# Kernel tuning notes

Hardware: AMD Instinct MI355X
Metric: run time of the kernel (lower is better)

Reference implementation:

```python
import jax, jax.numpy as jnp
import numpy as np

N = 100000   # nodes
E = 1600000  # directed edges
D_IN, D_HID, D_OUT, N_CLS = 128, 256, 128, 10
EPS = 1e-5


def gcn_conv(x, W, b, src, dst, n):
    # PyG GCNConv: h = XW, add self loops, sym-normalize, scatter-add to dst, + bias
    h = x @ W
    loop = jnp.arange(n)
    src_f = jnp.concatenate([src, loop])
    dst_f = jnp.concatenate([dst, loop])
    deg = jax.ops.segment_sum(jnp.ones(src_f.shape[0], h.dtype), dst_f, num_segments=n)
    dinv = jnp.where(deg > 0, jax.lax.rsqrt(deg), jnp.zeros_like(deg))
    norm = dinv[src_f] * dinv[dst_f]                    # [E+N]
    out = jax.ops.segment_sum(h[src_f] * norm[:, None], dst_f, num_segments=n)
    return out + b


def batchnorm(x, gamma, beta):
    # training-mode BatchNorm1d (batch statistics, biased variance)
    mu = x.mean(0)
    var = x.var(0)
    return gamma * (x - mu) * jax.lax.rsqrt(var + EPS) + beta


def setup_inputs() -> dict:
    key = jax.random.key(0)
    ks = jax.random.split(key, 12)
    x = jax.random.normal(ks[0], (N, D_IN), jnp.float32)
    edge_index = jax.random.randint(ks[1], (2, E), 0, N, dtype=jnp.int64)
    def lin(k, fi, fo):
        s = 1.0 / np.sqrt(fi)
        return jax.random.uniform(k, (fi, fo), jnp.float32, -s, s)
    return {
        "x": x, "edge_index": edge_index,
        "W1": lin(ks[2], D_IN, D_HID), "b1": jnp.zeros(D_HID, jnp.float32),
        "g1": jnp.ones(D_HID, jnp.float32), "beta1": jnp.zeros(D_HID, jnp.float32),
        "W2": lin(ks[3], D_HID, D_HID), "b2": jnp.zeros(D_HID, jnp.float32),
        "g2": jnp.ones(D_HID, jnp.float32), "beta2": jnp.zeros(D_HID, jnp.float32),
        "W3": lin(ks[4], D_HID, D_OUT), "b3": jnp.zeros(D_OUT, jnp.float32),
        "g3": jnp.ones(D_OUT, jnp.float32), "beta3": jnp.zeros(D_OUT, jnp.float32),
        "Wout": lin(ks[5], D_OUT, N_CLS), "bout": jnp.zeros(N_CLS, jnp.float32),
    }


def reference(x, edge_index, W1, b1, g1, beta1, W2, b2, g2, beta2,
              W3, b3, g3, beta3, Wout, bout):
    src, dst = edge_index[0], edge_index[1]
    h = jax.nn.relu(batchnorm(gcn_conv(x, W1, b1, src, dst, N), g1, beta1))
    h = jax.nn.relu(batchnorm(gcn_conv(h, W2, b2, src, dst, N), g2, beta2))
    h = jax.nn.relu(batchnorm(gcn_conv(h, W3, b3, src, dst, N), g3, beta3))
    return h @ Wout + bout
```

## Files before the change

### kernel.cpp

```cpp
#include <hip/hip_runtime.h>
#include <hip/hip_fp16.h>
#include <cstdint>
#include <cstddef>

#define EPS_BN 1e-5f
#define NSLICE 16
#define NCHUNK 16

static inline int cdiv(int a, int b) { return (a + b - 1) / b; }

using half8   = __attribute__((ext_vector_type(8))) _Float16;
using floatx4 = __attribute__((ext_vector_type(4))) float;

__device__ __forceinline__ float atomAddF(float* p, float v) {
    return unsafeAtomicAdd(p, v);
}


__global__ __launch_bounds__(256) void k_hist(const int* __restrict__ dst, int E,
                                              int NBLK, int NBUCK, int* __restrict__ H) {
    __shared__ int h[256];
    int t = threadIdx.x;
    h[t] = 0;
    __syncthreads();
    int base = blockIdx.x * 4096;
#pragma unroll
    for (int j = 0; j < 16; ++j) {
        int e = base + j * 256 + t;
        if (e < E) atomicAdd(&h[dst[e] >> 9], 1);
    }
    __syncthreads();
    if (t < NBUCK) H[t * NBLK + blockIdx.x] = h[t];
}

__global__ __launch_bounds__(256) void k_scan_reduce(const int* __restrict__ in, int m,
                                                     int* __restrict__ bsum) {
    int base = blockIdx.x * 1024;
    int t = threadIdx.x;
    int s = 0;
#pragma unroll
    for (int i = 0; i < 4; ++i) {
        int idx = base + t * 4 + i;
        if (idx < m) s += in[idx];
    }
    __shared__ int sm[256];
    sm[t] = s;
    __syncthreads();
    for (int off = 128; off > 0; off >>= 1) {
        if (t < off) sm[t] += sm[t + off];
        __syncthreads();
    }
    if (t == 0) bsum[blockIdx.x] = sm[0];
}

__global__ void k_scan_bsum(int* __restrict__ bsum, int nb) {
    if (threadIdx.x == 0 && blockIdx.x == 0) {
        int acc = 0;
        for (int i = 0; i < nb; ++i) { int v = bsum[i]; bsum[i] = acc; acc += v; }
    }
}

__global__ __launch_bounds__(256) void k_scan_final(const int* __restrict__ in, int m,
                                                    const int* __restrict__ bsum,
                                                    int* __restrict__ outS) {
    int base = blockIdx.x * 1024;
    int t = threadIdx.x;
    int v[4];
    int s = 0;
#pragma unroll
    for (int i = 0; i < 4; ++i) {
        int idx = base + t * 4 + i;
        v[i] = (idx < m) ? in[idx] : 0;
        s += v[i];
    }
    __shared__ int sm[256];
    sm[t] = s;
    __syncthreads();
    for (int off = 1; off < 256; off <<= 1) {
        int x = (t >= off) ? sm[t - off] : 0;
        __syncthreads();
        sm[t] += x;
        __syncthreads();
    }
    int excl = sm[t] - s + bsum[blockIdx.x];
#pragma unroll
    for (int i = 0; i < 4; ++i) {
        int idx = base + t * 4 + i;
        if (idx < m) { outS[idx] = excl; excl += v[i]; }
    }
}

__global__ __launch_bounds__(256) void k_bucket(const int* __restrict__ src,
                                                const int* __restrict__ dst, int E,
                                                int NBLK, int NBUCK,
                                                const int* __restrict__ S,
                                                unsigned* __restrict__ pairs) {
    __shared__ int cur[256];
    int t = threadIdx.x;
    if (t < NBUCK) cur[t] = S[t * NBLK + blockIdx.x];
    __syncthreads();
    int base = blockIdx.x * 4096;
#pragma unroll
    for (int j = 0; j < 16; ++j) {
        int e = base + j * 256 + t;
        if (e < E) {
            unsigned s = (unsigned)src[e];
            unsigned d = (unsigned)dst[e];
            int p = atomicAdd(&cur[d >> 9], 1);
            pairs[p] = ((d & 511u) << 17) | s;
        }
    }
}

__global__ __launch_bounds__(256) void k_build(const unsigned* __restrict__ pairs,
                                               const int* __restrict__ S,
                                               int NBLK, int NBUCK, int n, int E, int sh,
                                               int* __restrict__ endoff,
                                               float* __restrict__ dinv,
                                               int* __restrict__ csr) {
    int b = blockIdx.x;
    int nbase = b << 9;
    int bstart = S[b * NBLK];
    int bend = (b == NBUCK - 1) ? E : S[(b + 1) * NBLK];
    int t = threadIdx.x;
    __shared__ int sdeg[8192];
    __shared__ int scur[8192];
    __shared__ int stmp[256];
#pragma unroll
    for (int i = 0; i < 32; ++i) sdeg[t + i * 256] = 0;
    __syncthreads();
    for (int e = bstart + t; e < bend; e += 256) {
        unsigned p = pairs[e];
        int key = (int)((p >> 17) << 4) | (int)((p & 0x1FFFFu) >> sh);
        atomicAdd(&sdeg[key], 1);
    }
    __syncthreads();
    int loc[32];
    int ls = 0;
#pragma unroll
    for (int i = 0; i < 32; ++i) { loc[i] = sdeg[t * 32 + i]; ls += loc[i]; }
    stmp[t] = ls;
    __syncthreads();
    for (int off = 1; off < 256; off <<= 1) {
        int x = (t >= off) ? stmp[t - off] : 0;
        __syncthreads();
        stmp[t] += x;
        __syncthreads();
    }
    int run = bstart + stmp[t] - ls;
    int d0 = 0, d1 = 0;
    int v0 = nbase + 2 * t, v1 = v0 + 1;
#pragma unroll
    for (int i = 0; i < 32; ++i) {
        scur[t * 32 + i] = run;
        int e_ = run + loc[i];
        int v = (i < 16) ? v0 : v1;
        if (v < n) endoff[(size_t)v * NCHUNK + (i & 15)] = e_;
        run = e_;
        if (i < 16) d0 += loc[i]; else d1 += loc[i];
    }
    if (v0 < n) dinv[v0] = rsqrtf((float)(d0 + 1));
    if (v1 < n) dinv[v1] = rsqrtf((float)(d1 + 1));
    __syncthreads();
    for (int e = bstart + t; e < bend; e += 256) {
        unsigned p = pairs[e];
        int key = (int)((p >> 17) << 4) | (int)((p & 0x1FFFFu) >> sh);
        int pos = atomicAdd(&scur[key], 1);
        csr[pos] = (int)(p & 0x1FFFFu);
    }
}

__global__ __launch_bounds__(256) void k_prep(const float* __restrict__ x,
                                              const float* __restrict__ dinv,
                                              const float* __restrict__ W1,
                                              const float* __restrict__ W2,
                                              const float* __restrict__ W3,
                                              __half* __restrict__ xh,
                                              __half* __restrict__ Wt1,
                                              __half* __restrict__ Wt2,
                                              __half* __restrict__ Wt3,
                                              float* __restrict__ stats, int n) {
    int idx = blockIdx.x * 256 + threadIdx.x;
    int nx = n * 16;
    if (idx < nx) {
        int row = idx >> 4;
        float dv = dinv[row];
        const float4* p = (const float4*)x + (size_t)idx * 2;
        float4 a = p[0], b = p[1];
        uint4 o; __half2* oh = (__half2*)&o;
        oh[0] = __floats2half2_rn(a.x * dv, a.y * dv);
        oh[1] = __floats2half2_rn(a.z * dv, a.w * dv);
        oh[2] = __floats2half2_rn(b.x * dv, b.y * dv);
        oh[3] = __floats2half2_rn(b.z * dv, b.w * dv);
        ((uint4*)xh)[idx] = o;
        return;
    }
    int r = idx - nx;
    if (r < 32768) {
        int k = r >> 8, c = r & 255;
        Wt1[c * 128 + k] = __float2half(W1[r]);
    } else if (r < 98304) {
        int r2 = r - 32768;
        int k = r2 >> 8, c = r2 & 255;
        Wt2[c * 256 + k] = __float2half(W2[r2]);
    } else if (r < 131072) {
        int r2 = r - 98304;
        int k = r2 >> 7, c = r2 & 127;
        Wt3[c * 256 + k] = __float2half(W3[r2]);
    } else if (r < 131072 + NSLICE * 256 * 6) {
        stats[r - 131072] = 0.f;
    }
}

__device__ __forceinline__ void acc8(float* acc, uint4 d) {
    const __half2* h = (const __half2*)&d;
#pragma unroll
    for (int j = 0; j < 4; ++j) {
        float2 f = __half22float2(h[j]);
        acc[2 * j] += f.x; acc[2 * j + 1] += f.y;
    }
}

template<int D>
__device__ __forceinline__ void gseg(const __half* __restrict__ Pb,
                                     const int* __restrict__ csr,
                                     int i, int end, float* acc) {
    int rem = (end - i) & 3;
    if (rem & 2) {
        uint4 d0 = *(const uint4*)(Pb + (size_t)csr[i] * D);
        uint4 d1 = *(const uint4*)(Pb + (size_t)csr[i + 1] * D);
        acc8(acc, d0); acc8(acc, d1);
        i += 2;
    }
    if (rem & 1) {
        uint4 d0 = *(const uint4*)(Pb + (size_t)csr[i] * D);
        acc8(acc, d0);
        ++i;
    }
    if (i < end) {
        uint4 a[4];
#pragma unroll
        for (int u = 0; u < 4; ++u)
            a[u] = *(const uint4*)(Pb + (size_t)csr[i + u] * D);
        for (i += 4; i < end; i += 4) {
            uint4 b[4];
#pragma unroll
            for (int u = 0; u < 4; ++u)
                b[u] = *(const uint4*)(Pb + (size_t)csr[i + u] * D);
#pragma unroll
            for (int u = 0; u < 4; ++u) acc8(acc, a[u]);
#pragma unroll
            for (int u = 0; u < 4; ++u) a[u] = b[u];
        }
#pragma unroll
        for (int u = 0; u < 4; ++u) acc8(acc, a[u]);
    }
}

template<int D, bool STATS>
__global__ __launch_bounds__(256, 8) void k_gather4(const int* __restrict__ csr,
                                                    const int* __restrict__ endoff,
                                                    const __half* __restrict__ P,
                                                    const float* __restrict__ dinv,
                                                    __half* __restrict__ S, int n,
                                                    float* __restrict__ sums,
                                                    float* __restrict__ sqs) {
    constexpr int NSL = D / 64;
    __shared__ float red[STATS ? 2048 : 1];
    int bid = blockIdx.x;
    int x8 = bid & 7;
    int slice, gidx;
    if (NSL == 4) { slice = x8 >> 1; gidx = (bid >> 3) * 2 + (x8 & 1); }
    else          { slice = x8 >> 2; gidx = (bid >> 3) * 4 + (x8 & 3); }
    int Gn = (n + 31) >> 5;
    if (gidx >= Gn) return;
    int t = threadIdx.x;
    int lane = t & 7;
    int sub = t >> 3;
    int v = gidx * 32 + sub;
    int c0 = (int)((wall_clock64() / 100ull) & (unsigned long long)(NCHUNK - 1));
    const __half* Pb = P + (size_t)slice * 64 + lane * 8;
    float ov[8];
#pragma unroll
    for (int j = 0; j < 8; ++j) ov[j] = 0.f;
    if (v < n) {
        float acc[8];
        {
            uint4 d = *(const uint4*)(Pb + (size_t)v * D);
            const __half2* h = (const __half2*)&d;
#pragma unroll
            for (int j = 0; j < 4; ++j) {
                float2 f = __half22float2(h[j]);
                acc[2 * j] = f.x; acc[2 * j + 1] = f.y;
            }
        }
        size_t i0 = (size_t)v * NCHUNK;
        int beg = (i0 == 0) ? 0 : endoff[i0 - 1];
        int end = endoff[i0 + NCHUNK - 1];
        int mid = (c0 == 0) ? beg : endoff[i0 + c0 - 1];
        gseg<D>(Pb, csr, mid, end, acc);
        gseg<D>(Pb, csr, beg, mid, acc);
        float dv = dinv[v];
        uint4 o; __half2* oh = (__half2*)&o;
#pragma unroll
        for (int j = 0; j < 4; ++j) {
            float a0 = acc[2 * j] * dv, a1 = acc[2 * j + 1] * dv;
            oh[j] = __floats2half2_rn(a0, a1);
            ov[2 * j] = a0; ov[2 * j + 1] = a1;
        }
        *(uint4*)(S + (size_t)v * D + slice * 64 + lane * 8) = o;
    }
    if (STATS) {
        int shard = bid & (NSLICE - 1);
#pragma unroll
        for (int j = 0; j < 8; ++j) red[t * 8 + j] = ov[j];
        __syncthreads();
        if (t < 64) {
            int ln = t >> 3, j = t & 7;
            float ts = 0.f;
#pragma unroll
            for (int s = 0; s < 32; ++s) ts += red[(s * 8 + ln) * 8 + j];
            atomAddF(&sums[shard * 256 + slice * 64 + t], ts);
        }
        __syncthreads();
#pragma unroll
        for (int j = 0; j < 8; ++j) red[t * 8 + j] = ov[j] * ov[j];
        __syncthreads();
        if (t < 64) {
            int ln = t >> 3, j = t & 7;
            float tq = 0.f;
#pragma unroll
            for (int s = 0; s < 32; ++s) tq += red[(s * 8 + ln) * 8 + j];
            atomAddF(&sqs[shard * 256 + slice * 64 + t], tq);
        }
    }
}

template<int K, int NC, bool SCALE, bool BNIN, bool STATS>
__global__ __launch_bounds__(256) void k_gemm_mfma(const __half* __restrict__ A,
                                                   const __half* __restrict__ Wt,
                                                   const float* __restrict__ dinv,
                                                   const float* __restrict__ isum,
                                                   const float* __restrict__ isq,
                                                   const float* __restrict__ g,
                                                   const float* __restrict__ beta,
                                                   float* __restrict__ osum,
                                                   float* __restrict__ osq,
                                                   __half* __restrict__ C, int n) {
    constexpr int LDA = 40;
    __shared__ _Float16 As[128 * LDA];
    __shared__ _Float16 Bs[128 * LDA];
    __shared__ float ssc[BNIN ? K : 1];
    __shared__ float ssh[BNIN ? K : 1];
    __shared__ float scs[STATS ? 128 : 1];
    __shared__ float scq[STATS ? 128 : 1];
    int tid = threadIdx.x;
    if (BNIN) {
        float nf = (float)n;
        for (int i = tid; i < K; i += 256) {
            float su = 0.f, sq = 0.f;
#pragma unroll
            for (int s = 0; s < NSLICE; ++s) {
                su += isum[s * 256 + i];
                sq += isq[s * 256 + i];
            }
            float mu = su / nf;
            float var = sq / nf - mu * mu;
            float sc = g[i] * rsqrtf(var + EPS_BN);
            ssc[i] = sc; ssh[i] = beta[i] - mu * sc;
        }
        __syncthreads();
    }
    int wave = tid >> 6, lane = tid & 63;
    int wr = wave >> 1, wc = wave & 1;
    int q = lane >> 4, l16 = lane & 15;
    int row0 = blockIdx.x * 128;
    int col0 = blockIdx.y * 128;
    floatx4 acc[4][4];
#pragma unroll
    for (int r = 0; r < 4; ++r)
#pragma unroll
        for (int c = 0; c < 4; ++c) acc[r][c] = (floatx4)0.0f;

    for (int k0 = 0; k0 < K; k0 += 32) {
#pragma unroll
        for (int i = 0; i < 2; ++i) {
            int s = tid + i * 256;
            int r = s >> 2, ks = s & 3;
            uint4 d = *(const uint4*)(A + (size_t)(row0 + r) * K + k0 + ks * 8);
            if (BNIN) {
                const __half2* h = (const __half2*)&d;
                uint4 o; __half2* oh = (__half2*)&o;
                int kb = k0 + ks * 8;
#pragma unroll
                for (int j = 0; j < 4; ++j) {
                    float2 f = __half22float2(h[j]);
                    float y0 = fmaxf(0.f, f.x * ssc[kb + 2 * j]     + ssh[kb + 2 * j]);
                    float y1 = fmaxf(0.f, f.y * ssc[kb + 2 * j + 1] + ssh[kb + 2 * j + 1]);
                    oh[j] = __floats2half2_rn(y0, y1);
                }
                d = o;
            }
            *(uint4*)&As[r * LDA + ks * 8] = d;
        }
#pragma unroll
        for (int i = 0; i < 2; ++i) {
            int s = tid + i * 256;
            int r = s >> 2, ks = s & 3;
            uint4 d = *(const uint4*)(Wt + (size_t)(col0 + r) * K + k0 + ks * 8);
            *(uint4*)&Bs[r * LDA + ks * 8] = d;
        }
        __syncthreads();
        half8 af[4], bf[4];
#pragma unroll
        for (int r = 0; r < 4; ++r)
            af[r] = *(const half8*)&As[(wr * 64 + r * 16 + l16) * LDA + q * 8];
#pragma unroll
        for (int c = 0; c < 4; ++c)
            bf[c] = *(const half8*)&Bs[(wc * 64 + c * 16 + l16) * LDA + q * 8];
#pragma unroll
        for (int r = 0; r < 4; ++r)
#pragma unroll
            for (int c = 0; c < 4; ++c)
                acc[r][c] = __builtin_amdgcn_mfma_f32_16x16x32_f16(af[r], bf[c], acc[r][c], 0, 0, 0);
        __syncthreads();
    }
    float colsum[4] = {};
    float colsq[4]  = {};
#pragma unroll
    for (int r = 0; r < 4; ++r) {
#pragma unroll
        for (int reg = 0; reg < 4; ++reg) {
            int grow = row0 + wr * 64 + r * 16 + q * 4 + reg;
            float sc = 1.f;
            if (SCALE) sc = (grow < n) ? dinv[grow] : 0.f;
            __half* cp = C + (size_t)grow * NC + col0 + wc * 64 + l16;
#pragma unroll
            for (int c = 0; c < 4; ++c) {
                float v = acc[r][c][reg] * sc;
                cp[c * 16] = __float2half(v);
                if (STATS && grow < n) { colsum[c] += v; colsq[c] += v * v; }
            }
        }
    }
    if (STATS) {
        if (tid < 128) { scs[tid] = 0.f; scq[tid] = 0.f; }
        __syncthreads();
#pragma unroll
        for (int c = 0; c < 4; ++c) {
            atomicAdd(&scs[wc * 64 + c * 16 + l16], colsum[c]);
            atomicAdd(&scq[wc * 64 + c * 16 + l16], colsq[c]);
        }
        __syncthreads();
        if (tid < 128) {
            int slice = blockIdx.x & (NSLICE - 1);
            atomAddF(&osum[slice * 256 + col0 + tid], scs[tid]);
            atomAddF(&osq[slice * 256 + col0 + tid], scq[tid]);
        }
    }
}

__global__ __launch_bounds__(256) void k_out(const __half* __restrict__ H,
                                             const float* __restrict__ sums,
                                             const float* __restrict__ sqs,
                                             const float* __restrict__ g,
                                             const float* __restrict__ beta,
                                             const float* __restrict__ Wout,
                                             const float* __restrict__ bout,
                                             float* __restrict__ out, int n) {
    __shared__ float Wl[128 * 10];
    __shared__ float bl[10];
    __shared__ float osc[128];
    __shared__ float osh[128];
    __shared__ float red[256 * 10];
    int tid = threadIdx.x;
    for (int i = tid; i < 1280; i += 256) Wl[i] = Wout[i];
    if (tid < 10) bl[tid] = bout[tid];
    if (tid < 128) {
        float nf = (float)n;
        float su = 0.f, sq = 0.f;
#pragma unroll
        for (int s = 0; s < NSLICE; ++s) {
            su += sums[s * 256 + tid];
            sq += sqs[s * 256 + tid];
        }
        float mu = su / nf;
        float var = sq / nf - mu * mu;
        float sc = g[tid] * rsqrtf(var + EPS_BN);
        osc[tid] = sc; osh[tid] = beta[tid] - mu * sc;
    }
    __syncthreads();
    int rl = tid >> 1;
    int h2 = tid & 1;
    int r = blockIdx.x * 128 + rl;
    float p[10] = {};
    if (r < n) {
        const __half* a = H + (size_t)r * 128 + h2 * 64;
#pragma unroll 8
        for (int k = 0; k < 64; ++k) {
            int col = h2 * 64 + k;
            float av = fmaxf(0.f, __half2float(a[k]) * osc[col] + osh[col]);
            const float* wr = Wl + col * 10;
#pragma unroll
            for (int c = 0; c < 10; ++c) p[c] += av * wr[c];
        }
    }
    float* rr = red + (size_t)tid * 10;
#pragma unroll
    for (int c = 0; c < 10; ++c) rr[c] = p[c];
    __syncthreads();
    if (h2 == 0 && r < n) {
        const float* rb = red + (size_t)tid * 10;
#pragma unroll
        for (int c = 0; c < 10; ++c) {
            out[(size_t)r * 10 + c] = rb[c] + rb[10 + c] + bl[c];
        }
    }
}

extern "C" void kernel_launch(void* const* d_in, const int* in_sizes, int n_in,
                              void* d_out, int out_size, void* d_ws, size_t ws_size,
                              hipStream_t stream) {
    const float* x    = (const float*)d_in[0];
    const int*   ei   = (const int*)d_in[1];
    const float* W1   = (const float*)d_in[2];
    const float* g1   = (const float*)d_in[4];
    const float* be1  = (const float*)d_in[5];
    const float* W2   = (const float*)d_in[6];
    const float* g2   = (const float*)d_in[8];
    const float* be2  = (const float*)d_in[9];
    const float* W3   = (const float*)d_in[10];
    const float* g3   = (const float*)d_in[12];
    const float* be3  = (const float*)d_in[13];
    const float* Wout = (const float*)d_in[14];
    const float* bout = (const float*)d_in[15];
    float* out = (float*)d_out;

    int n = in_sizes[0] / 128;
    int E = in_sizes[1] / 2;
    const int* esrc = ei;
    const int* edst = ei + E;
    int npad = cdiv(n, 128) * 128;
    int NBLK = cdiv(E, 4096);
    int NBUCK = (n + 511) >> 9;
    if (NBUCK > 256) return;
    int m = NBUCK * NBLK;
    int nb2 = cdiv(m, 1024);
    int sh = 0;
    while ((NCHUNK << sh) < n) ++sh;

    const size_t align = 256;
    auto al = [&](size_t s) { return (s + align - 1) & ~(align - 1); };
    size_t n4  = al((size_t)n * 4 + 512);
    size_t nE8 = al((size_t)n * NCHUNK * 4 + 512);

    const size_t statsLayer = (size_t)NSLICE * 256 * 2 * 4;
    const size_t statsTotal = statsLayer * 3;

    char* ws = (char*)d_ws;
    size_t o_end   = 0;
    size_t o_dinv  = o_end + nE8;
    size_t o_stats = o_dinv + n4;
    size_t o_bsum  = o_stats + statsTotal;
    size_t o_H     = o_bsum + 1024;
    size_t o_Hs    = o_H + al((size_t)m * 4);
    size_t o_csr   = o_Hs + al((size_t)m * 4);
    size_t o_pairs = o_csr + al((size_t)E * 4);
    size_t o_w1    = o_pairs + al((size_t)E * 4);
    size_t o_w2    = o_w1 + al(256 * 128 * 2);
    size_t o_w3    = o_w2 + al(256 * 256 * 2);
    size_t o_A128a = o_w3 + al(128 * 256 * 2);
    size_t o_A128b = o_A128a + al((size_t)npad * 128 * 2);
    size_t o_A256a = o_A128b + al((size_t)npad * 128 * 2);
    size_t o_A256b = o_A256a + al((size_t)npad * 256 * 2);
    size_t need    = o_A256b + (size_t)npad * 256 * 2;
    if (ws_size < need) return;

    int*      endoff = (int*)(ws + o_end);
    float*    dinv   = (float*)(ws + o_dinv);
    float*    stats  = (float*)(ws + o_stats);
    float*    sums1  = stats;
    float*    sqs1   = sums1 + NSLICE * 256;
    float*    sums2  = (float*)(ws + o_stats + statsLayer);
    float*    sqs2   = sums2 + NSLICE * 256;
    float*    sums3  = (float*)(ws + o_stats + 2 * statsLayer);
    float*    sqs3   = sums3 + NSLICE * 256;
    int*      bsum   = (int*)(ws + o_bsum);
    int*      H      = (int*)(ws + o_H);
    int*      Hs     = (int*)(ws + o_Hs);
    int*      csr    = (int*)(ws + o_csr);
    unsigned* pairs  = (unsigned*)(ws + o_pairs);
    __half*   Wt1    = (__half*)(ws + o_w1);
    __half*   Wt2    = (__half*)(ws + o_w2);
    __half*   Wt3    = (__half*)(ws + o_w3);
    __half*   xh     = (__half*)(ws + o_A128a);
    __half*   S3     = (__half*)(ws + o_A128a);
    __half*   G1     = (__half*)(ws + o_A128b);
    __half*   P3     = (__half*)(ws + o_A128b);
    __half*   P1     = (__half*)(ws + o_A256a);
    __half*   S2     = (__half*)(ws + o_A256a);
    __half*   P2     = (__half*)(ws + o_A256b);

    k_hist<<<NBLK, 256, 0, stream>>>(edst, E, NBLK, NBUCK, H);
    k_scan_reduce<<<nb2, 256, 0, stream>>>(H, m, bsum);
    k_scan_bsum<<<1, 64, 0, stream>>>(bsum, nb2);
    k_scan_final<<<nb2, 256, 0, stream>>>(H, m, bsum, Hs);
    k_bucket<<<NBLK, 256, 0, stream>>>(esrc, edst, E, NBLK, NBUCK, Hs, pairs);
    k_build<<<NBUCK, 256, 0, stream>>>(pairs, Hs, NBLK, NBUCK, n, E, sh, endoff, dinv, csr);

    int prepTotal = n * 16 + 131072 + NSLICE * 256 * 6;
    k_prep<<<cdiv(prepTotal, 256), 256, 0, stream>>>(
        x, dinv, W1, W2, W3, xh, Wt1, Wt2, Wt3, stats, n);

    int Gn = (n + 31) >> 5;
    int grid128 = 8 * cdiv(Gn, 4);
    int grid256 = 8 * cdiv(Gn, 2);

    k_gather4<128, false><<<grid128, 256, 0, stream>>>(
        csr, endoff, xh, dinv, G1, n, nullptr, nullptr);
    k_gemm_mfma<128, 256, false, false, true><<<dim3(npad / 128, 2), 256, 0, stream>>>(
        G1, Wt1, dinv, nullptr, nullptr, nullptr, nullptr, sums1, sqs1, P1, n);

    k_gemm_mfma<256, 256, true, true, false><<<dim3(npad / 128, 2), 256, 0, stream>>>(
        P1, Wt2, dinv, sums1, sqs1, g1, be1, nullptr, nullptr, P2, n);
    k_gather4<256, true><<<grid256, 256, 0, stream>>>(
        csr, endoff, P2, dinv, S2, n, sums2, sqs2);

    k_gemm_mfma<256, 128, true, true, false><<<dim3(npad / 128, 1), 256, 0, stream>>>(
        S2, Wt3, dinv, sums2, sqs2, g2, be2, nullptr, nullptr, P3, n);
    k_gather4<128, true><<<grid128, 256, 0, stream>>>(
        csr, endoff, P3, dinv, S3, n, sums3, sqs3);

    k_out<<<cdiv(n, 128), 256, 0, stream>>>(S3, sums3, sqs3, g3, be3, Wout, bout, out, n);
}
```

Before: 539.1 us.

## Fold self-loops into CSR and widen GEMM blocks to full output width

Self-loop edges are now appended as synthetic edges during histogram and bucketing, so the CSR includes them. Degree no longer adds one explicitly, and the gather drops its separate self-row load. Separately, the MFMA GEMM now computes all NC output columns in one block of 2*NC threads instead of splitting columns across a second grid dimension, so each A tile is loaded and BN-transformed once. The costs are more edges to sort and gather (E+n) and fewer, larger GEMM blocks.

```diff
diff --git a/kernel.cpp b/kernel.cpp
--- a/kernel.cpp
+++ b/kernel.cpp
@@ -17,7 +17,7 @@
 }
 
 
-__global__ __launch_bounds__(256) void k_hist(const int* __restrict__ dst, int E,
+__global__ __launch_bounds__(256) void k_hist(const int* __restrict__ dst, int E, int EL,
                                               int NBLK, int NBUCK, int* __restrict__ H) {
     __shared__ int h[256];
     int t = threadIdx.x;
@@ -27,7 +27,10 @@
 #pragma unroll
     for (int j = 0; j < 16; ++j) {
         int e = base + j * 256 + t;
-        if (e < E) atomicAdd(&h[dst[e] >> 9], 1);
+        if (e < EL) {
+            int d = (e < E) ? dst[e] : (e - E);
+            atomicAdd(&h[d >> 9], 1);
+        }
     }
     __syncthreads();
     if (t < NBUCK) H[t * NBLK + blockIdx.x] = h[t];
@@ -91,7 +94,7 @@
 }
 
 __global__ __launch_bounds__(256) void k_bucket(const int* __restrict__ src,
-                                                const int* __restrict__ dst, int E,
+                                                const int* __restrict__ dst, int E, int EL,
                                                 int NBLK, int NBUCK,
                                                 const int* __restrict__ S,
                                                 unsigned* __restrict__ pairs) {
@@ -103,9 +106,10 @@
 #pragma unroll
     for (int j = 0; j < 16; ++j) {
         int e = base + j * 256 + t;
-        if (e < E) {
-            unsigned s = (unsigned)src[e];
-            unsigned d = (unsigned)dst[e];
+        if (e < EL) {
+            unsigned s, d;
+            if (e < E) { s = (unsigned)src[e]; d = (unsigned)dst[e]; }
+            else       { s = d = (unsigned)(e - E); }
             int p = atomicAdd(&cur[d >> 9], 1);
             pairs[p] = ((d & 511u) << 17) | s;
         }
@@ -114,14 +118,14 @@
 
 __global__ __launch_bounds__(256) void k_build(const unsigned* __restrict__ pairs,
                                                const int* __restrict__ S,
-                                               int NBLK, int NBUCK, int n, int E, int sh,
+                                               int NBLK, int NBUCK, int n, int EL, int sh,
                                                int* __restrict__ endoff,
                                                float* __restrict__ dinv,
                                                int* __restrict__ csr) {
     int b = blockIdx.x;
     int nbase = b << 9;
     int bstart = S[b * NBLK];
-    int bend = (b == NBUCK - 1) ? E : S[(b + 1) * NBLK];
+    int bend = (b == NBUCK - 1) ? EL : S[(b + 1) * NBLK];
     int t = threadIdx.x;
     __shared__ int sdeg[8192];
     __shared__ int scur[8192];
@@ -159,8 +163,8 @@
         run = e_;
         if (i < 16) d0 += loc[i]; else d1 += loc[i];
     }
-    if (v0 < n) dinv[v0] = rsqrtf((float)(d0 + 1));
-    if (v1 < n) dinv[v1] = rsqrtf((float)(d1 + 1));
+    if (v0 < n) dinv[v0] = rsqrtf((float)d0);
+    if (v1 < n) dinv[v1] = rsqrtf((float)d1);
     __syncthreads();
     for (int e = bstart + t; e < bend; e += 256) {
         unsigned p = pairs[e];
@@ -258,7 +262,7 @@
 }
 
 template<int D, bool STATS>
-__global__ __launch_bounds__(256, 8) void k_gather4(const int* __restrict__ csr,
+__global__ __launch_bounds__(256, 8) void k_gather6(const int* __restrict__ csr,
                                                     const int* __restrict__ endoff,
                                                     const __half* __restrict__ P,
                                                     const float* __restrict__ dinv,
@@ -284,16 +288,7 @@
 #pragma unroll
     for (int j = 0; j < 8; ++j) ov[j] = 0.f;
     if (v < n) {
-        float acc[8];
-        {
-            uint4 d = *(const uint4*)(Pb + (size_t)v * D);
-            const __half2* h = (const __half2*)&d;
-#pragma unroll
-            for (int j = 0; j < 4; ++j) {
-                float2 f = __half22float2(h[j]);
-                acc[2 * j] = f.x; acc[2 * j + 1] = f.y;
-            }
-        }
+        float acc[8] = {};
         size_t i0 = (size_t)v * NCHUNK;
         int beg = (i0 == 0) ? 0 : endoff[i0 - 1];
         int end = endoff[i0 + NCHUNK - 1];
@@ -337,7 +332,7 @@
 }
 
 template<int K, int NC, bool SCALE, bool BNIN, bool STATS>
-__global__ __launch_bounds__(256) void k_gemm_mfma(const __half* __restrict__ A,
+__global__ __launch_bounds__(2 * NC) void k_gemm_mfma(const __half* __restrict__ A,
                                                    const __half* __restrict__ Wt,
                                                    const float* __restrict__ dinv,
                                                    const float* __restrict__ isum,
@@ -347,17 +342,19 @@
                                                    float* __restrict__ osum,
                                                    float* __restrict__ osq,
                                                    __half* __restrict__ C, int n) {
+    constexpr int THREADS = 2 * NC;
+    constexpr int CW = NC / 64;
     constexpr int LDA = 40;
     __shared__ _Float16 As[128 * LDA];
-    __shared__ _Float16 Bs[128 * LDA];
+    __shared__ _Float16 Bs[NC * LDA];
     __shared__ float ssc[BNIN ? K : 1];
     __shared__ float ssh[BNIN ? K : 1];
-    __shared__ float scs[STATS ? 128 : 1];
-    __shared__ float scq[STATS ? 128 : 1];
+    __shared__ float scs[STATS ? NC : 1];
+    __shared__ float scq[STATS ? NC : 1];
     int tid = threadIdx.x;
     if (BNIN) {
         float nf = (float)n;
-        for (int i = tid; i < K; i += 256) {
+        for (int i = tid; i < K; i += THREADS) {
             float su = 0.f, sq = 0.f;
 #pragma unroll
             for (int s = 0; s < NSLICE; ++s) {
@@ -372,10 +369,9 @@
         __syncthreads();
     }
     int wave = tid >> 6, lane = tid & 63;
-    int wr = wave >> 1, wc = wave & 1;
+    int wr = wave / CW, wc = wave % CW;
     int q = lane >> 4, l16 = lane & 15;
     int row0 = blockIdx.x * 128;
-    int col0 = blockIdx.y * 128;
     floatx4 acc[4][4];
 #pragma unroll
     for (int r = 0; r < 4; ++r)
@@ -383,9 +379,10 @@
         for (int c = 0; c < 4; ++c) acc[r][c] = (floatx4)0.0f;
 
     for (int k0 = 0; k0 < K; k0 += 32) {
-#pragma unroll
-        for (int i = 0; i < 2; ++i) {
-            int s = tid + i * 256;
+        constexpr int AIT = 512 / THREADS;
+#pragma unroll
+        for (int i = 0; i < AIT; ++i) {
+            int s = tid + i * THREADS;
             int r = s >> 2, ks = s & 3;
             uint4 d = *(const uint4*)(A + (size_t)(row0 + r) * K + k0 + ks * 8);
             if (BNIN) {
@@ -403,11 +400,12 @@
             }
             *(uint4*)&As[r * LDA + ks * 8] = d;
         }
-#pragma unroll
-        for (int i = 0; i < 2; ++i) {
-            int s = tid + i * 256;
+        constexpr int BIT = NC * 4 / THREADS;
+#pragma unroll
+        for (int i = 0; i < BIT; ++i) {
+            int s = tid + i * THREADS;
             int r = s >> 2, ks = s & 3;
-            uint4 d = *(const uint4*)(Wt + (size_t)(col0 + r) * K + k0 + ks * 8);
+            uint4 d = *(const uint4*)(Wt + (size_t)r * K + k0 + ks * 8);
             *(uint4*)&Bs[r * LDA + ks * 8] = d;
         }
         __syncthreads();
@@ -434,7 +432,7 @@
             int grow = row0 + wr * 64 + r * 16 + q * 4 + reg;
             float sc = 1.f;
             if (SCALE) sc = (grow < n) ? dinv[grow] : 0.f;
-            __half* cp = C + (size_t)grow * NC + col0 + wc * 64 + l16;
+            __half* cp = C + (size_t)grow * NC + wc * 64 + l16;
 #pragma unroll
             for (int c = 0; c < 4; ++c) {
                 float v = acc[r][c][reg] * sc;
@@ -444,7 +442,7 @@
         }
     }
     if (STATS) {
-        if (tid < 128) { scs[tid] = 0.f; scq[tid] = 0.f; }
+        if (tid < NC) { scs[tid] = 0.f; scq[tid] = 0.f; }
         __syncthreads();
 #pragma unroll
         for (int c = 0; c < 4; ++c) {
@@ -452,10 +450,10 @@
             atomicAdd(&scq[wc * 64 + c * 16 + l16], colsq[c]);
         }
         __syncthreads();
-        if (tid < 128) {
+        if (tid < NC) {
             int slice = blockIdx.x & (NSLICE - 1);
-            atomAddF(&osum[slice * 256 + col0 + tid], scs[tid]);
-            atomAddF(&osq[slice * 256 + col0 + tid], scq[tid]);
+            atomAddF(&osum[slice * 256 + tid], scs[tid]);
+            atomAddF(&osq[slice * 256 + tid], scq[tid]);
         }
     }
 }
@@ -540,8 +538,9 @@
     int E = in_sizes[1] / 2;
     const int* esrc = ei;
     const int* edst = ei + E;
+    int EL = E + n;
     int npad = cdiv(n, 128) * 128;
-    int NBLK = cdiv(E, 4096);
+    int NBLK = cdiv(EL, 4096);
     int NBUCK = (n + 511) >> 9;
     if (NBUCK > 256) return;
     int m = NBUCK * NBLK;
@@ -565,8 +564,8 @@
     size_t o_H     = o_bsum + 1024;
     size_t o_Hs    = o_H + al((size_t)m * 4);
     size_t o_csr   = o_Hs + al((size_t)m * 4);
-    size_t o_pairs = o_csr + al((size_t)E * 4);
-    size_t o_w1    = o_pairs + al((size_t)E * 4);
+    size_t o_pairs = o_csr + al((size_t)EL * 4);
+    size_t o_w1    = o_pairs + al((size_t)EL * 4);
     size_t o_w2    = o_w1 + al(256 * 128 * 2);
     size_t o_w3    = o_w2 + al(256 * 256 * 2);
     size_t o_A128a = o_w3 + al(128 * 256 * 2);
@@ -601,12 +600,12 @@
     __half*   S2     = (__half*)(ws + o_A256a);
     __half*   P2     = (__half*)(ws + o_A256b);
 
-    k_hist<<<NBLK, 256, 0, stream>>>(edst, E, NBLK, NBUCK, H);
+    k_hist<<<NBLK, 256, 0, stream>>>(edst, E, EL, NBLK, NBUCK, H);
     k_scan_reduce<<<nb2, 256, 0, stream>>>(H, m, bsum);
     k_scan_bsum<<<1, 64, 0, stream>>>(bsum, nb2);
     k_scan_final<<<nb2, 256, 0, stream>>>(H, m, bsum, Hs);
-    k_bucket<<<NBLK, 256, 0, stream>>>(esrc, edst, E, NBLK, NBUCK, Hs, pairs);
-    k_build<<<NBUCK, 256, 0, stream>>>(pairs, Hs, NBLK, NBUCK, n, E, sh, endoff, dinv, csr);
+    k_bucket<<<NBLK, 256, 0, stream>>>(esrc, edst, E, EL, NBLK, NBUCK, Hs, pairs);
+    k_build<<<NBUCK, 256, 0, stream>>>(pairs, Hs, NBLK, NBUCK, n, EL, sh, endoff, dinv, csr);
 
     int prepTotal = n * 16 + 131072 + NSLICE * 256 * 6;
     k_prep<<<cdiv(prepTotal, 256), 256, 0, stream>>>(
@@ -616,19 +615,19 @@
     int grid128 = 8 * cdiv(Gn, 4);
     int grid256 = 8 * cdiv(Gn, 2);
 
-    k_gather4<128, false><<<grid128, 256, 0, stream>>>(
+    k_gather6<128, false><<<grid128, 256, 0, stream>>>(
         csr, endoff, xh, dinv, G1, n, nullptr, nullptr);
-    k_gemm_mfma<128, 256, false, false, true><<<dim3(npad / 128, 2), 256, 0, stream>>>(
+    k_gemm_mfma<128, 256, false, false, true><<<dim3(npad / 128), 512, 0, stream>>>(
         G1, Wt1, dinv, nullptr, nullptr, nullptr, nullptr, sums1, sqs1, P1, n);
 
-    k_gemm_mfma<256, 256, true, true, false><<<dim3(npad / 128, 2), 256, 0, stream>>>(
+    k_gemm_mfma<256, 256, true, true, false><<<dim3(npad / 128), 512, 0, stream>>>(
         P1, Wt2, dinv, sums1, sqs1, g1, be1, nullptr, nullptr, P2, n);
-    k_gather4<256, true><<<grid256, 256, 0, stream>>>(
+    k_gather6<256, true><<<grid256, 256, 0, stream>>>(
         csr, endoff, P2, dinv, S2, n, sums2, sqs2);
 
-    k_gemm_mfma<256, 128, true, true, false><<<dim3(npad / 128, 1), 256, 0, stream>>>(
+    k_gemm_mfma<256, 128, true, true, false><<<dim3(npad / 128), 256, 0, stream>>>(
         S2, Wt3, dinv, sums2, sqs2, g2, be2, nullptr, nullptr, P3, n);
-    k_gather4<128, true><<<grid128, 256, 0, stream>>>(
+    k_gather6<128, true><<<grid128, 256, 0, stream>>>(
         csr, endoff, P3, dinv, S3, n, sums3, sqs3);
 
     k_out<<<cdiv(n, 128), 256, 0, stream>>>(S3, sums3, sqs3, g3, be3, Wout, bout, out, n);
```

New measurement: 540.0 us (median of 2 runs). About the same (+0.2%).
